# Performance work log

Measured on AMD Instinct MI355X. Metric: run time of the kernel, lower is better.

## Reference

```python
import jax, jax.numpy as jnp
import numpy as np

B, S, D = 2, 2048, 1024
H = 16
HD = D // H


def setup_inputs() -> dict:
    key = jax.random.key(0)
    ks = jax.random.split(key, 6)
    x = jax.random.normal(ks[0], (B, S, D), dtype=jnp.float32)
    scale = 1.0 / np.sqrt(D)
    Wq = jax.random.normal(ks[1], (D, D), dtype=jnp.float32) * scale
    Wk = jax.random.normal(ks[2], (D, D), dtype=jnp.float32) * scale
    Wv = jax.random.normal(ks[3], (D, D), dtype=jnp.float32) * scale
    Wo = jax.random.normal(ks[4], (D, D), dtype=jnp.float32) * scale
    bo = jax.random.normal(ks[5], (D,), dtype=jnp.float32) * 0.01
    return {"x": x, "Wq": Wq, "Wk": Wk, "Wv": Wv, "Wo": Wo, "bo": bo}


def reference(x, Wq, Wk, Wv, Wo, bo):
    b, t, _ = x.shape
    # QKV projections (no bias), split into heads: [b, h, t, hd]
    q = (x @ Wq).reshape(b, t, H, HD).transpose(0, 2, 1, 3)
    k = (x @ Wk).reshape(b, t, H, HD).transpose(0, 2, 1, 3)
    v = (x @ Wv).reshape(b, t, H, HD).transpose(0, 2, 1, 3)
    # scores [b, h, t, t]; causal mask (upper triangle -> -inf) applied before scaling
    scores = jnp.einsum("bhqd,bhkd->bhqk", q, k)
    causal = jnp.triu(jnp.ones((t, t), dtype=bool), k=1)
    scores = jnp.where(causal, -jnp.inf, scores)
    attn = jax.nn.softmax(scores / jnp.sqrt(jnp.asarray(HD, scores.dtype)), axis=-1)
    ctx = jnp.einsum("bhqk,bhkd->bhqd", attn, v)
    ctx = ctx.transpose(0, 2, 1, 3).reshape(b, t, H * HD)
    return ctx @ Wo + bo
```

## Files before the change

### kernel.cpp

```cpp
#include <hip/hip_runtime.h>

#define B_ 2
#define S_ 2048
#define D_ 1024
#define H_ 16
#define HD_ 64
#define M_ (B_*S_)

typedef __attribute__((ext_vector_type(8))) short bf16x8;
typedef __attribute__((ext_vector_type(4))) short s16x4;
typedef __attribute__((ext_vector_type(4))) float f32x4;
typedef __attribute__((ext_vector_type(4))) unsigned int u32x4;

static __device__ __forceinline__ unsigned short f2bf(float f) {
  unsigned int u = __builtin_bit_cast(unsigned int, f);
  u += 0x7FFFu + ((u >> 16) & 1u);
  return (unsigned short)(u >> 16);
}

static __device__ __forceinline__ unsigned int cvt_pk_bf16(float a, float b) {
  unsigned int r;
  asm("v_cvt_pk_bf16_f32 %0, %1, %2" : "=v"(r) : "v"(a), "v"(b));
  return r;
}

static __device__ __forceinline__ void gload_lds16(const void* g, void* l) {
  __builtin_amdgcn_global_load_lds(
      (const __attribute__((address_space(1))) unsigned int*)g,
      (__attribute__((address_space(3))) unsigned int*)l, 16, 0, 0);
}

__global__ __launch_bounds__(256) void xcvt_kernel(const float* __restrict__ x,
                                                   unsigned short* __restrict__ xb) {
  size_t i = ((size_t)blockIdx.x * 256 + threadIdx.x) * 8;
  float4 a = ((const float4*)(x + i))[0];
  float4 b = ((const float4*)(x + i))[1];
  bf16x8 w;
  w[0]=(short)f2bf(a.x); w[1]=(short)f2bf(a.y); w[2]=(short)f2bf(a.z); w[3]=(short)f2bf(a.w);
  w[4]=(short)f2bf(b.x); w[5]=(short)f2bf(b.y); w[6]=(short)f2bf(b.z); w[7]=(short)f2bf(b.w);
  *(bf16x8*)(xb + i) = w;
}

__global__ void wtrans_kernel(const float* __restrict__ Wq, const float* __restrict__ Wk,
                              const float* __restrict__ Wv, const float* __restrict__ Wo,
                              unsigned short* __restrict__ wt) {
  __shared__ float tile[32][33];
  const float* W = blockIdx.z==0 ? Wq : blockIdx.z==1 ? Wk : blockIdx.z==2 ? Wv : Wo;
  unsigned short* out = wt + (size_t)blockIdx.z * D_ * D_;
  int n0 = blockIdx.x*32, k0 = blockIdx.y*32;
  int tx = threadIdx.x, ty = threadIdx.y;
  #pragma unroll
  for (int i=0;i<4;i++) tile[ty+i*8][tx] = W[(size_t)(k0+ty+i*8)*D_ + n0+tx];
  __syncthreads();
  #pragma unroll
  for (int i=0;i<4;i++) out[(size_t)(n0+ty+i*8)*D_ + (k0+tx)] = f2bf(tile[tx][ty+i*8]);
}

#define GEMM_K_LOOP(Abase, Bbase)                                                     \
  for (int ks = 0; ks < 16; ++ks) {                                                   \
    const int k0 = ks * 64;                                                           \
    __syncthreads();                                                                  \
    _Pragma("unroll")                                                                 \
    for (int p = 0; p < 4; ++p) {                                                     \
      int c = p*256 + t;                                                              \
      int row = c >> 3, sl = (c & 7) ^ (row & 7);                                     \
      gload_lds16(Abase + (size_t)row*D_ + k0 + sl*8, &As[(p*256 + wid*64)*8]);       \
    }                                                                                 \
    _Pragma("unroll")                                                                 \
    for (int p = 0; p < 4; ++p) {                                                     \
      int c = p*256 + t;                                                              \
      int row = c >> 3, sl = (c & 7) ^ (row & 7);                                     \
      gload_lds16(Bbase + (size_t)row*D_ + k0 + sl*8, &Bs[(p*256 + wid*64)*8]);       \
    }                                                                                 \
    __syncthreads();                                                                  \
    _Pragma("unroll")                                                                 \
    for (int kk = 0; kk < 2; ++kk) {                                                  \
      bf16x8 af[4], bfr[4];                                                           \
      _Pragma("unroll")                                                               \
      for (int m = 0; m < 4; ++m) {                                                   \
        int row = wr + m*16 + l15;                                                    \
        af[m] = *(const bf16x8*)((const char*)As + row*128 + (((kk*4+lg)^(row&7))<<4)); \
      }                                                                               \
      _Pragma("unroll")                                                               \
      for (int n = 0; n < 4; ++n) {                                                   \
        int row = wc + n*16 + l15;                                                    \
        bfr[n] = *(const bf16x8*)((const char*)Bs + row*128 + (((kk*4+lg)^(row&7))<<4)); \
      }                                                                               \
      _Pragma("unroll")                                                               \
      for (int m = 0; m < 4; ++m)                                                     \
        _Pragma("unroll")                                                             \
        for (int n = 0; n < 4; ++n)                                                   \
          acc[m][n] = __builtin_amdgcn_mfma_f32_16x16x32_bf16(af[m], bfr[n], acc[m][n], 0,0,0); \
    }                                                                                 \
  }

__global__ __launch_bounds__(256,3) void gemm_qkv_kernel(
    const unsigned short* __restrict__ xb, const unsigned short* __restrict__ wt,
    unsigned short* __restrict__ Qo, unsigned short* __restrict__ Ko,
    unsigned short* __restrict__ Vto) {
  __shared__ __align__(16) unsigned short As[128*64];
  __shared__ __align__(16) unsigned short Bs[128*64];
  const int z = blockIdx.z;
  const int m0 = blockIdx.y*128, n0 = blockIdx.x*128;
  const int t = threadIdx.x, lane = t & 63, wid = t >> 6;
  const int wr = (wid>>1)*64, wc = (wid&1)*64;
  const int l15 = lane & 15, lg = lane >> 4;
  const unsigned short* Ab = xb + (size_t)m0 * D_;
  const unsigned short* Bb = wt + (size_t)z * D_ * D_ + (size_t)n0 * D_;

  f32x4 acc[4][4];
  #pragma unroll
  for (int m=0;m<4;m++)
    #pragma unroll
    for (int n=0;n<4;n++) acc[m][n] = f32x4{0.f,0.f,0.f,0.f};

  GEMM_K_LOOP(Ab, Bb)

  const float qscale = 0.18033688011112042f;
  #pragma unroll
  for (int m=0;m<4;m++) {
    #pragma unroll
    for (int n=0;n<4;n++) {
      #pragma unroll
      for (int r=0;r<4;r++) {
        int gm = m0 + wr + m*16 + lg*4 + r;
        int gn = n0 + wc + n*16 + l15;
        int b = gm >> 11, s = gm & (S_-1);
        int h = gn >> 6,  d = gn & 63;
        float av = acc[m][n][r];
        if (z==0) av *= qscale;
        unsigned short val = f2bf(av);
        if (z==0)      Qo[(((size_t)(b*H_+h))*S_ + s)*HD_ + d] = val;
        else if (z==1) Ko[(((size_t)(b*H_+h))*S_ + s)*HD_ + d] = val;
        else           Vto[(((size_t)(b*H_+h))*HD_ + d)*S_ + s] = val;
      }
    }
  }
}

__global__ __launch_bounds__(256,4) void attn_kernel(
    const unsigned short* __restrict__ Q, const unsigned short* __restrict__ K,
    const unsigned short* __restrict__ Vt, unsigned short* __restrict__ ctx) {
  __shared__ __align__(16) unsigned short KT[2][64*64];
  __shared__ __align__(16) unsigned short VT[2][64*64];
  const int t = threadIdx.x, lane = t & 63, wid = t >> 6;
  const int bh = blockIdx.x & 31;
  const int qt = 31 - (int)(blockIdx.x >> 5);
  const int b = bh >> 4, h = bh & 15;
  const int qw0 = qt*64 + wid*16;
  const int nchunk = qt + 1;
  const unsigned short* Qp = Q  + (size_t)bh * S_ * HD_;
  const unsigned short* Kp = K  + (size_t)bh * S_ * HD_;
  const unsigned short* Vp = Vt + (size_t)bh * HD_ * S_;
  const int l15 = lane & 15, lg = lane >> 4;
  const int rsub = lane >> 3, slot = lane & 7;
  const int sslot = slot ^ rsub;

  bf16x8 qf0 = *(const bf16x8*)(Qp + (size_t)(qw0 + l15)*HD_ + lg*8);
  bf16x8 qf1 = *(const bf16x8*)(Qp + (size_t)(qw0 + l15)*HD_ + 32 + lg*8);

  f32x4 o[4];
  #pragma unroll
  for (int dt=0;dt<4;dt++) o[dt] = f32x4{0.f,0.f,0.f,0.f};
  f32x4 accl = f32x4{0.f,0.f,0.f,0.f};
  s16x4 ones;
  ones[0] = (short)0x3F80; ones[1] = (short)0x3F80;
  ones[2] = (short)0x3F80; ones[3] = (short)0x3F80;

  const unsigned short* kS0 = Kp + (size_t)(16*wid + rsub)*HD_ + sslot*8;
  const unsigned short* kS1 = kS0 + 8*HD_;
  const unsigned short* vS0 = Vp + (size_t)(16*wid + rsub)*S_ + sslot*8;
  const unsigned short* vS1 = vS0 + 8*S_;

  auto stage = [&](int buf) {
    unsigned short* kd = &KT[buf][16*wid*64];
    unsigned short* vd = &VT[buf][16*wid*64];
    gload_lds16(kS0, kd);
    gload_lds16(kS1, kd + 8*64);
    gload_lds16(vS0, vd);
    gload_lds16(vS1, vd + 8*64);
    kS0 += 64*HD_; kS1 += 64*HD_;
    vS0 += 64;     vS1 += 64;
  };

  auto body = [&](int cur, bool domask) {
    const char* Kt = (const char*)&KT[cur][0];
    const char* Vv = (const char*)&VT[cur][0];

    f32x4 st[4];
    __builtin_amdgcn_s_setprio(1);
    #pragma unroll
    for (int kt=0; kt<4; ++kt) {
      int row = kt*16 + l15;
      int sw = (row & 7) << 4;
      bf16x8 kf0 = *(const bf16x8*)(Kt + row*128 + ((lg*16)      ^ sw));
      bf16x8 kf1 = *(const bf16x8*)(Kt + row*128 + ((64 + lg*16) ^ sw));
      f32x4 z = f32x4{0.f,0.f,0.f,0.f};
      z = __builtin_amdgcn_mfma_f32_16x16x32_bf16(kf0, qf0, z, 0,0,0);
      z = __builtin_amdgcn_mfma_f32_16x16x32_bf16(kf1, qf1, z, 0,0,0);
      st[kt] = z;
    }
    __builtin_amdgcn_s_setprio(0);

    if (domask) {
      const int qloc = wid*16 + l15;
      #pragma unroll
      for (int kt=0;kt<4;kt++)
        #pragma unroll
        for (int r=0;r<4;r++)
          if (kt*16 + lg*4 + r > qloc) st[kt][r] = -INFINITY;
    }

    s16x4 pa[4];
    #pragma unroll
    for (int kt=0;kt<4;kt++) {
      float p0 = exp2f(st[kt][0]);
      float p1 = exp2f(st[kt][1]);
      float p2 = exp2f(st[kt][2]);
      float p3 = exp2f(st[kt][3]);
      uint2 u;
      u.x = cvt_pk_bf16(p0, p1);
      u.y = cvt_pk_bf16(p2, p3);
      pa[kt] = __builtin_bit_cast(s16x4, u);
    }

    __builtin_amdgcn_s_setprio(1);
    #pragma unroll
    for (int kt=0;kt<4;kt++)
      accl = __builtin_amdgcn_mfma_f32_16x16x16bf16_1k(pa[kt], ones, accl, 0,0,0);
    #pragma unroll
    for (int dt=0;dt<4;dt++) {
      int row = dt*16 + l15;
      int sw = (row & 7) << 4;
      const char* vrow = Vv + row*128;
      #pragma unroll
      for (int kt=0;kt<4;kt++) {
        s16x4 vb = *(const s16x4*)(vrow + ((kt*32 + lg*8) ^ sw));
        o[dt] = __builtin_amdgcn_mfma_f32_16x16x16bf16_1k(pa[kt], vb, o[dt], 0,0,0);
      }
    }
    __builtin_amdgcn_s_setprio(0);
  };

  stage(0);
  __syncthreads();

  int cur = 0;
  for (int ch=0; ch<nchunk-1; ++ch) {
    stage(cur^1);
    body(cur, false);
    __syncthreads();
    cur ^= 1;
  }
  body(cur, true);

  float lr[4];
  #pragma unroll
  for (int r=0;r<4;r++) lr[r] = 1.f / accl[r];
  #pragma unroll
  for (int dt=0;dt<4;dt++)
    #pragma unroll
    for (int r=0;r<4;r++) {
      size_t row = (size_t)(b*S_ + qw0 + lg*4 + r);
      ctx[row*D_ + h*HD_ + dt*16 + l15] = f2bf(o[dt][r] * lr[r]);
    }
}

__global__ __launch_bounds__(256,3) void gemm_out_kernel(
    const unsigned short* __restrict__ ctx, const unsigned short* __restrict__ WtO,
    const float* __restrict__ bo, float* __restrict__ out) {
  __shared__ __align__(16) unsigned short As[128*64];
  __shared__ __align__(16) unsigned short Bs[128*64];
  const int m0 = blockIdx.y*128, n0 = blockIdx.x*128;
  const int t = threadIdx.x, lane = t & 63, wid = t >> 6;
  const int wr = (wid>>1)*64, wc = (wid&1)*64;
  const int l15 = lane & 15, lg = lane >> 4;
  const unsigned short* Ab = ctx + (size_t)m0 * D_;
  const unsigned short* Bb = WtO + (size_t)n0 * D_;

  f32x4 acc[4][4];
  #pragma unroll
  for (int m=0;m<4;m++)
    #pragma unroll
    for (int n=0;n<4;n++) acc[m][n] = f32x4{0.f,0.f,0.f,0.f};

  GEMM_K_LOOP(Ab, Bb)

  #pragma unroll
  for (int n=0;n<4;n++) {
    float bias = bo[n0 + wc + n*16 + l15];
    #pragma unroll
    for (int m=0;m<4;m++)
      #pragma unroll
      for (int r=0;r<4;r++) {
        int gm = m0 + wr + m*16 + lg*4 + r;
        int gn = n0 + wc + n*16 + l15;
        out[(size_t)gm*D_ + gn] = acc[m][n][r] + bias;
      }
  }
}

extern "C" void kernel_launch(void* const* d_in, const int* in_sizes, int n_in,
                              void* d_out, int out_size, void* d_ws, size_t ws_size,
                              hipStream_t stream) {
  (void)in_sizes; (void)n_in; (void)out_size; (void)ws_size;
  const float* x  = (const float*)d_in[0];
  const float* Wq = (const float*)d_in[1];
  const float* Wk = (const float*)d_in[2];
  const float* Wv = (const float*)d_in[3];
  const float* Wo = (const float*)d_in[4];
  const float* bo = (const float*)d_in[5];
  float* out = (float*)d_out;

  unsigned short* wt  = (unsigned short*)d_ws;
  unsigned short* Qb  = wt  + (size_t)4*D_*D_;
  unsigned short* Kb  = Qb  + (size_t)M_*D_;
  unsigned short* Vtb = Kb  + (size_t)M_*D_;
  unsigned short* ctb = Vtb + (size_t)M_*D_;
  unsigned short* xbb = ctb + (size_t)M_*D_;

  xcvt_kernel<<<dim3(M_*D_/(256*8)), 256, 0, stream>>>(x, xbb);
  wtrans_kernel<<<dim3(32,32,4), dim3(32,8), 0, stream>>>(Wq, Wk, Wv, Wo, wt);
  gemm_qkv_kernel<<<dim3(8,32,3), 256, 0, stream>>>(xbb, wt, Qb, Kb, Vtb);
  attn_kernel<<<dim3(1024), 256, 0, stream>>>(Qb, Kb, Vtb, ctb);
  gemm_out_kernel<<<dim3(8,32), 256, 0, stream>>>(ctb, wt + (size_t)3*D_*D_, bo, out);
}
```

Baseline: 115.5 us.

## Split attention KV dimension across waves with LDS tree reduction of partial outputs

Each wave now owns a 16-key slice of every KV chunk for all 64 query rows, instead of owning 16 query rows over all keys. Each wave therefore loads only its own K and V fragments from LDS once per chunk, rather than every wave reading the full tile. The partial O and row-sum accumulators are then combined through a two-step LDS tree reduction before wave 0 normalises and writes the output. The cost is four times as many accumulator registers (occupancy hint lowered from 4 to 3), extra barriers, and a serial epilogue in which only wave 0 stores results.

```diff
diff --git a/kernel.cpp b/kernel.cpp
--- a/kernel.cpp
+++ b/kernel.cpp
@@ -138,16 +138,17 @@
   }
 }
 
-__global__ __launch_bounds__(256,4) void attn_kernel(
+__global__ __launch_bounds__(256,3) void attn_kernel(
     const unsigned short* __restrict__ Q, const unsigned short* __restrict__ K,
     const unsigned short* __restrict__ Vt, unsigned short* __restrict__ ctx) {
   __shared__ __align__(16) unsigned short KT[2][64*64];
   __shared__ __align__(16) unsigned short VT[2][64*64];
+  __shared__ float LS[2][64];
   const int t = threadIdx.x, lane = t & 63, wid = t >> 6;
   const int bh = blockIdx.x & 31;
   const int qt = 31 - (int)(blockIdx.x >> 5);
   const int b = bh >> 4, h = bh & 15;
-  const int qw0 = qt*64 + wid*16;
+  const int q0 = qt * 64;
   const int nchunk = qt + 1;
   const unsigned short* Qp = Q  + (size_t)bh * S_ * HD_;
   const unsigned short* Kp = K  + (size_t)bh * S_ * HD_;
@@ -156,13 +157,21 @@
   const int rsub = lane >> 3, slot = lane & 7;
   const int sslot = slot ^ rsub;
 
-  bf16x8 qf0 = *(const bf16x8*)(Qp + (size_t)(qw0 + l15)*HD_ + lg*8);
-  bf16x8 qf1 = *(const bf16x8*)(Qp + (size_t)(qw0 + l15)*HD_ + 32 + lg*8);
-
-  f32x4 o[4];
-  #pragma unroll
-  for (int dt=0;dt<4;dt++) o[dt] = f32x4{0.f,0.f,0.f,0.f};
-  f32x4 accl = f32x4{0.f,0.f,0.f,0.f};
+  bf16x8 qf0[4], qf1[4];
+  #pragma unroll
+  for (int j=0;j<4;j++) {
+    qf0[j] = *(const bf16x8*)(Qp + (size_t)(q0 + j*16 + l15)*HD_ + lg*8);
+    qf1[j] = *(const bf16x8*)(Qp + (size_t)(q0 + j*16 + l15)*HD_ + 32 + lg*8);
+  }
+
+  f32x4 o[4][4];
+  f32x4 accl[4];
+  #pragma unroll
+  for (int j=0;j<4;j++) {
+    accl[j] = f32x4{0.f,0.f,0.f,0.f};
+    #pragma unroll
+    for (int dt=0;dt<4;dt++) o[j][dt] = f32x4{0.f,0.f,0.f,0.f};
+  }
   s16x4 ones;
   ones[0] = (short)0x3F80; ones[1] = (short)0x3F80;
   ones[2] = (short)0x3F80; ones[3] = (short)0x3F80;
@@ -183,62 +192,64 @@
     vS0 += 64;     vS1 += 64;
   };
 
+  const int krow = wid*16 + l15;
+  const int ksw = (krow & 7) << 4;
+
   auto body = [&](int cur, bool domask) {
     const char* Kt = (const char*)&KT[cur][0];
     const char* Vv = (const char*)&VT[cur][0];
 
+    bf16x8 kf0 = *(const bf16x8*)(Kt + krow*128 + ((lg*16)      ^ ksw));
+    bf16x8 kf1 = *(const bf16x8*)(Kt + krow*128 + ((64 + lg*16) ^ ksw));
+    s16x4 vb[4];
+    #pragma unroll
+    for (int dt=0;dt<4;dt++) {
+      int vrow = dt*16 + l15;
+      int vsw = (vrow & 7) << 4;
+      vb[dt] = *(const s16x4*)(Vv + vrow*128 + ((wid*32 + lg*8) ^ vsw));
+    }
+
     f32x4 st[4];
     __builtin_amdgcn_s_setprio(1);
     #pragma unroll
-    for (int kt=0; kt<4; ++kt) {
-      int row = kt*16 + l15;
-      int sw = (row & 7) << 4;
-      bf16x8 kf0 = *(const bf16x8*)(Kt + row*128 + ((lg*16)      ^ sw));
-      bf16x8 kf1 = *(const bf16x8*)(Kt + row*128 + ((64 + lg*16) ^ sw));
+    for (int j=0;j<4;j++) {
       f32x4 z = f32x4{0.f,0.f,0.f,0.f};
-      z = __builtin_amdgcn_mfma_f32_16x16x32_bf16(kf0, qf0, z, 0,0,0);
-      z = __builtin_amdgcn_mfma_f32_16x16x32_bf16(kf1, qf1, z, 0,0,0);
-      st[kt] = z;
+      z = __builtin_amdgcn_mfma_f32_16x16x32_bf16(kf0, qf0[j], z, 0,0,0);
+      z = __builtin_amdgcn_mfma_f32_16x16x32_bf16(kf1, qf1[j], z, 0,0,0);
+      st[j] = z;
     }
     __builtin_amdgcn_s_setprio(0);
 
     if (domask) {
-      const int qloc = wid*16 + l15;
-      #pragma unroll
-      for (int kt=0;kt<4;kt++)
-        #pragma unroll
-        for (int r=0;r<4;r++)
-          if (kt*16 + lg*4 + r > qloc) st[kt][r] = -INFINITY;
+      #pragma unroll
+      for (int j=0;j<4;j++)
+        #pragma unroll
+        for (int r=0;r<4;r++)
+          if (wid*16 + lg*4 + r > j*16 + l15) st[j][r] = -INFINITY;
     }
 
     s16x4 pa[4];
     #pragma unroll
-    for (int kt=0;kt<4;kt++) {
-      float p0 = exp2f(st[kt][0]);
-      float p1 = exp2f(st[kt][1]);
-      float p2 = exp2f(st[kt][2]);
-      float p3 = exp2f(st[kt][3]);
+    for (int j=0;j<4;j++) {
+      float p0 = exp2f(st[j][0]);
+      float p1 = exp2f(st[j][1]);
+      float p2 = exp2f(st[j][2]);
+      float p3 = exp2f(st[j][3]);
       uint2 u;
       u.x = cvt_pk_bf16(p0, p1);
       u.y = cvt_pk_bf16(p2, p3);
-      pa[kt] = __builtin_bit_cast(s16x4, u);
+      pa[j] = __builtin_bit_cast(s16x4, u);
     }
 
     __builtin_amdgcn_s_setprio(1);
     #pragma unroll
-    for (int kt=0;kt<4;kt++)
-      accl = __builtin_amdgcn_mfma_f32_16x16x16bf16_1k(pa[kt], ones, accl, 0,0,0);
-    #pragma unroll
-    for (int dt=0;dt<4;dt++) {
-      int row = dt*16 + l15;
-      int sw = (row & 7) << 4;
-      const char* vrow = Vv + row*128;
-      #pragma unroll
-      for (int kt=0;kt<4;kt++) {
-        s16x4 vb = *(const s16x4*)(vrow + ((kt*32 + lg*8) ^ sw));
-        o[dt] = __builtin_amdgcn_mfma_f32_16x16x16bf16_1k(pa[kt], vb, o[dt], 0,0,0);
-      }
-    }
+    for (int j=0;j<4;j++)
+      accl[j] = __builtin_amdgcn_mfma_f32_16x16x16bf16_1k(pa[j], ones, accl[j], 0,0,0);
+    #pragma unroll
+    for (int j=0;j<4;j++)
+      #pragma unroll
+      for (int dt=0;dt<4;dt++)
+        o[j][dt] = __builtin_amdgcn_mfma_f32_16x16x16bf16_1k(pa[j], vb[dt], o[j][dt], 0,0,0);
     __builtin_amdgcn_s_setprio(0);
   };
 
@@ -254,16 +265,75 @@
   }
   body(cur, true);
 
-  float lr[4];
-  #pragma unroll
-  for (int r=0;r<4;r++) lr[r] = 1.f / accl[r];
-  #pragma unroll
-  for (int dt=0;dt<4;dt++)
-    #pragma unroll
-    for (int r=0;r<4;r++) {
-      size_t row = (size_t)(b*S_ + qw0 + lg*4 + r);
-      ctx[row*D_ + h*HD_ + dt*16 + l15] = f2bf(o[dt][r] * lr[r]);
-    }
+  float* bufA = (float*)&KT[0][0];
+  float* bufB = (float*)&VT[0][0];
+  __syncthreads();
+
+  if (wid & 1) {
+    float* dst = (wid == 1) ? bufA : bufB;
+    #pragma unroll
+    for (int j=0;j<4;j++) {
+      #pragma unroll
+      for (int dt=0;dt<4;dt++)
+        #pragma unroll
+        for (int r=0;r<4;r++)
+          dst[(j*16 + lg*4 + r)*64 + dt*16 + l15] = o[j][dt][r];
+      if (l15 == 0)
+        #pragma unroll
+        for (int r=0;r<4;r++) LS[wid>>1][j*16 + lg*4 + r] = accl[j][r];
+    }
+  }
+  __syncthreads();
+  if (!(wid & 1)) {
+    float* src = (wid == 0) ? bufA : bufB;
+    #pragma unroll
+    for (int j=0;j<4;j++) {
+      #pragma unroll
+      for (int dt=0;dt<4;dt++)
+        #pragma unroll
+        for (int r=0;r<4;r++)
+          o[j][dt][r] += src[(j*16 + lg*4 + r)*64 + dt*16 + l15];
+      #pragma unroll
+      for (int r=0;r<4;r++) accl[j][r] += LS[wid>>1][j*16 + lg*4 + r];
+    }
+  }
+  __syncthreads();
+  if (wid == 2) {
+    #pragma unroll
+    for (int j=0;j<4;j++) {
+      #pragma unroll
+      for (int dt=0;dt<4;dt++)
+        #pragma unroll
+        for (int r=0;r<4;r++)
+          bufA[(j*16 + lg*4 + r)*64 + dt*16 + l15] = o[j][dt][r];
+      if (l15 == 0)
+        #pragma unroll
+        for (int r=0;r<4;r++) LS[0][j*16 + lg*4 + r] = accl[j][r];
+    }
+  }
+  __syncthreads();
+  if (wid == 0) {
+    #pragma unroll
+    for (int j=0;j<4;j++) {
+      #pragma unroll
+      for (int dt=0;dt<4;dt++)
+        #pragma unroll
+        for (int r=0;r<4;r++)
+          o[j][dt][r] += bufA[(j*16 + lg*4 + r)*64 + dt*16 + l15];
+      #pragma unroll
+      for (int r=0;r<4;r++) accl[j][r] += LS[0][j*16 + lg*4 + r];
+      float lr[4];
+      #pragma unroll
+      for (int r=0;r<4;r++) lr[r] = 1.f / accl[j][r];
+      #pragma unroll
+      for (int dt=0;dt<4;dt++)
+        #pragma unroll
+        for (int r=0;r<4;r++) {
+          size_t row = (size_t)(b*S_ + q0 + j*16 + lg*4 + r);
+          ctx[row*D_ + h*HD_ + dt*16 + l15] = f2bf(o[j][dt][r] * lr[r]);
+        }
+    }
+  }
 }
 
 __global__ __launch_bounds__(256,3) void gemm_out_kernel(
```

Result: no change. 113.4 us (-1.8%).
